# Kernel tuning notes

Hardware: AMD Instinct MI355X
Metric: run time of the kernel (lower is better)

The kernel has to match this reference:

```python
import jax, jax.numpy as jnp
import numpy as np

B, T, C = 4, 2048, 1024
N_HEAD = 16
HEAD_DIM = C // N_HEAD


def setup_inputs() -> dict:
    key = jax.random.key(0)
    ks = jax.random.split(key, 5)
    scale = 0.02
    return {
        "x": jax.random.normal(ks[0], (B, T, C), dtype=jnp.float32),
        "w_attn": jax.random.normal(ks[1], (C, 3 * C), dtype=jnp.float32) * scale,
        "b_attn": jax.random.normal(ks[2], (3 * C,), dtype=jnp.float32) * scale,
        "w_proj": jax.random.normal(ks[3], (C, C), dtype=jnp.float32) * scale,
        "b_proj": jax.random.normal(ks[4], (C,), dtype=jnp.float32) * scale,
    }


def reference(x, w_attn, b_attn, w_proj, b_proj):
    Bq, Tq, Cq = x.shape
    qkv = x @ w_attn + b_attn  # [B, T, 3C]
    q, k, v = jnp.split(qkv, 3, axis=2)
    # [B, H, T, D]
    q = q.reshape(Bq, Tq, N_HEAD, HEAD_DIM).transpose(0, 2, 1, 3)
    k = k.reshape(Bq, Tq, N_HEAD, HEAD_DIM).transpose(0, 2, 1, 3)
    v = v.reshape(Bq, Tq, N_HEAD, HEAD_DIM).transpose(0, 2, 1, 3)
    att = jnp.einsum("bhqd,bhkd->bhqk", q, k) * (HEAD_DIM ** -0.5)
    causal = jnp.tril(jnp.ones((Tq, Tq), dtype=bool))
    att = jnp.where(causal[None, None, :, :], att, -jnp.inf)
    att = jax.nn.softmax(att, axis=-1)
    out = jnp.einsum("bhqk,bhkd->bhqd", att, v)  # [B, H, T, D]
    out = out.transpose(0, 2, 1, 3).reshape(Bq, Tq, Cq)
    return out @ w_proj + b_proj
```

## Files before the change

kernel.cpp:

```cpp
#include <hip/hip_runtime.h>
#include <hip/hip_bf16.h>

#define Bsz 4
#define Tsz 2048
#define Csz 1024
#define NH  16
#define HD  64
#define NT  (Bsz * Tsz)

typedef unsigned short u16;
typedef unsigned int   u32;
typedef u16   u16x8  __attribute__((ext_vector_type(8)));
typedef u16   u16x4  __attribute__((ext_vector_type(4)));
typedef u32   u32x2  __attribute__((ext_vector_type(2)));
typedef short s16x8  __attribute__((ext_vector_type(8)));
typedef float f32x4  __attribute__((ext_vector_type(4)));

__device__ __forceinline__ float b2f(u16 u) {
    union { unsigned int i; float f; } x; x.i = ((unsigned int)u) << 16; return x.f;
}
__device__ __forceinline__ u16 f2b(float f) {
    unsigned int u = __float_as_uint(f);
    return (u16)((u + 0x7FFF + ((u >> 16) & 1)) >> 16);
}
__device__ __forceinline__ float ex2(float x) {
    float r; asm("v_exp_f32 %0, %1" : "=v"(r) : "v"(x)); return r;
}
__device__ __forceinline__ u32 cvtpk(float lo, float hi) {
    u32 r; asm("v_cvt_pk_bf16_f32 %0, %1, %2" : "=v"(r) : "v"(lo), "v"(hi)); return r;
}
__device__ __forceinline__ void gload16(const u16* g, u16* l) {
    __builtin_amdgcn_global_load_lds(
        (const __attribute__((address_space(1))) void*)g,
        (__attribute__((address_space(3))) void*)l, 16, 0, 0);
}

__global__ __launch_bounds__(256)
void conv_f32_bf16(const float* __restrict__ in, u16* __restrict__ out, int n8)
{
    int t = blockIdx.x * 256 + threadIdx.x;
    if (t >= n8) return;
    const float4* p = reinterpret_cast<const float4*>(in) + (size_t)t * 2;
    float4 a = p[0], b = p[1];
    u16x8 w;
    w[0] = f2b(a.x); w[1] = f2b(a.y); w[2] = f2b(a.z); w[3] = f2b(a.w);
    w[4] = f2b(b.x); w[5] = f2b(b.y); w[6] = f2b(b.z); w[7] = f2b(b.w);
    *(reinterpret_cast<u16x8*>(out) + t) = w;
}

__global__ __launch_bounds__(256)
void transpose_conv(const float* __restrict__ in, u16* __restrict__ out, int K, int N)
{
    __shared__ float tile[32][33];
    const int n0 = blockIdx.x * 32, k0 = blockIdx.y * 32;
    const int tx = threadIdx.x & 31, ty = threadIdx.x >> 5;
#pragma unroll
    for (int j = 0; j < 4; ++j)
        tile[ty + j * 8][tx] = in[(size_t)(k0 + ty + j * 8) * N + n0 + tx];
    __syncthreads();
#pragma unroll
    for (int j = 0; j < 4; ++j)
        out[(size_t)(n0 + ty + j * 8) * K + k0 + tx] = f2b(tile[tx][ty + j * 8]);
}

template<typename OutT>
__global__ __launch_bounds__(256)
void gemm_bf16(const u16* __restrict__ A, const u16* __restrict__ Bt,
               const float* __restrict__ bias, OutT* __restrict__ C,
               int M, int N, int K)
{
    __shared__ u16 As[128 * 64];
    __shared__ u16 Bs[128 * 64];

    const int tid  = threadIdx.x;
    const int lane = tid & 63;
    const int wid  = tid >> 6;
    const int wr   = wid >> 1;
    const int wc   = wid & 1;
    const int g    = lane >> 4;
    const int rr   = lane & 15;
    const int srow = lane >> 3;
    const int sslt = lane & 7;

    const int n0 = blockIdx.x * 128;
    const int m0 = blockIdx.y * 128;

    f32x4 acc[4][4];
#pragma unroll
    for (int m = 0; m < 4; ++m)
#pragma unroll
        for (int n = 0; n < 4; ++n) acc[m][n] = (f32x4){0.f, 0.f, 0.f, 0.f};

    for (int k0 = 0; k0 < K; k0 += 64) {
        __syncthreads();
#pragma unroll
        for (int p = 0; p < 4; ++p) {
            const int q = p * 4 + wid;
            const int r = q * 8 + srow;
            gload16(A  + (size_t)(m0 + r) * K + k0 + sslt * 8, &As[q * 512]);
            gload16(Bt + (size_t)(n0 + r) * K + k0 + sslt * 8, &Bs[q * 512]);
        }
        __syncthreads();

#pragma unroll
        for (int kk = 0; kk < 2; ++kk) {
            s16x8 af[4], bfr[4];
            const int s = kk * 4 + g;
#pragma unroll
            for (int m = 0; m < 4; ++m)
                af[m] = *reinterpret_cast<const s16x8*>(
                    &As[(wr * 64 + m * 16 + rr) * 64 + s * 8]);
#pragma unroll
            for (int n = 0; n < 4; ++n)
                bfr[n] = *reinterpret_cast<const s16x8*>(
                    &Bs[(wc * 64 + n * 16 + rr) * 64 + s * 8]);
#pragma unroll
            for (int m = 0; m < 4; ++m)
#pragma unroll
                for (int n = 0; n < 4; ++n)
                    acc[m][n] = __builtin_amdgcn_mfma_f32_16x16x32_bf16(
                        af[m], bfr[n], acc[m][n], 0, 0, 0);
        }
    }

#pragma unroll
    for (int m = 0; m < 4; ++m) {
#pragma unroll
        for (int n = 0; n < 4; ++n) {
            const int col = n0 + wc * 64 + n * 16 + rr;
            const float bv = bias[col];
#pragma unroll
            for (int j = 0; j < 4; ++j) {
                const int row = m0 + wr * 64 + m * 16 + g * 4 + j;
                const float v = acc[m][n][j] + bv;
                if constexpr (sizeof(OutT) == 2)
                    C[(size_t)row * N + col] = (OutT)f2b(v);
                else
                    C[(size_t)row * N + col] = (OutT)v;
            }
        }
    }
}

__global__ __launch_bounds__(256)
void attn_mfma(const u16* __restrict__ qkv, u16* __restrict__ out)
{
    __shared__ __align__(128) u16 Ks[64 * 64];
    __shared__ __align__(128) u16 Vt[64 * 64];
    __shared__ __align__(128) u16 Pl[4 * 2048];

    const int tid  = threadIdx.x;
    const int lane = tid & 63;
    const int wid  = tid >> 6;
    const int c    = lane & 15;
    const int g    = lane >> 4;

    const int bh = blockIdx.x;
    const int b  = bh >> 4;
    const int h  = bh & 15;
    const int skey = tid >> 3;
    const int sb   = tid & 7;
    const u32 pbyte = ((u32)(size_t)(&Pl[0])) + wid * 4096 + lane * 8;
    const float QSC = 0.18033688f;

    for (int half = 0; half < 2; ++half) {
        const int yt = half ? 15 - (int)blockIdx.y : (int)blockIdx.y;
        const int t0 = yt * 128;
        const int qb0 = t0 + wid * 32;

        s16x8 qf[2][2];
#pragma unroll
        for (int m = 0; m < 2; ++m)
#pragma unroll
            for (int kk = 0; kk < 2; ++kk) {
                u16x8 raw = *reinterpret_cast<const u16x8*>(
                    qkv + (size_t)(b * Tsz + qb0 + m * 16 + c) * (3 * Csz)
                        + h * HD + kk * 32 + g * 8);
                s16x8 qv;
#pragma unroll
                for (int i = 0; i < 8; ++i) qv[i] = (short)f2b(b2f(raw[i]) * QSC);
                qf[m][kk] = qv;
            }

        f32x4 acco[2][4];
#pragma unroll
        for (int m = 0; m < 2; ++m)
#pragma unroll
            for (int dn = 0; dn < 4; ++dn) acco[m][dn] = (f32x4){0.f, 0.f, 0.f, 0.f};
        float mrun[8], lrun[8];
#pragma unroll
        for (int i = 0; i < 8; ++i) { mrun[i] = -1e30f; lrun[i] = 0.f; }

        for (int kt = 0; kt < t0 + 128; kt += 64) {
#pragma unroll
            for (int p = 0; p < 2; ++p) {
                const int key = skey + p * 32;
                const u16* gk = qkv + (size_t)(b * Tsz + kt + key) * (3 * Csz)
                                + Csz + h * HD + sb * 8;
                u16x8 kv = *reinterpret_cast<const u16x8*>(gk);
                u16x8 vv = *reinterpret_cast<const u16x8*>(gk + Csz);
                *reinterpret_cast<u16x8*>(&Ks[key * 64 + ((sb ^ (key & 7)) * 8)]) = kv;
#pragma unroll
                for (int i = 0; i < 8; ++i) {
                    const int d = sb * 8 + i;
                    Vt[d * 64 + (key ^ (((i ^ sb) & 7) << 3))] = vv[i];
                }
            }
            __syncthreads();

            if (kt <= qb0 + 31) {
                f32x4 accS[2][4];
#pragma unroll
                for (int m = 0; m < 2; ++m)
#pragma unroll
                    for (int n = 0; n < 4; ++n) accS[m][n] = (f32x4){0.f, 0.f, 0.f, 0.f};
#pragma unroll
                for (int kk = 0; kk < 2; ++kk) {
                    s16x8 kf[4];
#pragma unroll
                    for (int n = 0; n < 4; ++n) {
                        const int key = n * 16 + c;
                        kf[n] = *reinterpret_cast<const s16x8*>(
                            &Ks[key * 64 + (((kk * 4 + g) ^ (c & 7)) * 8)]);
                    }
#pragma unroll
                    for (int m = 0; m < 2; ++m)
#pragma unroll
                        for (int n = 0; n < 4; ++n)
                            accS[m][n] = __builtin_amdgcn_mfma_f32_16x16x32_bf16(
                                qf[m][kk], kf[n], accS[m][n], 0, 0, 0);
                }

                if (kt + 63 > qb0) {
#pragma unroll
                    for (int m = 0; m < 2; ++m)
#pragma unroll
                        for (int n = 0; n < 4; ++n) {
                            const int kgl = kt + n * 16 + c;
#pragma unroll
                            for (int j = 0; j < 4; ++j) {
                                const int qg = qb0 + m * 16 + g * 4 + j;
                                if (kgl > qg) accS[m][n][j] = -1e30f;
                            }
                        }
                }

                float pm[8];
#pragma unroll
                for (int m = 0; m < 2; ++m)
#pragma unroll
                    for (int j = 0; j < 4; ++j)
                        pm[m * 4 + j] = fmaxf(fmaxf(accS[m][0][j], accS[m][1][j]),
                                              fmaxf(accS[m][2][j], accS[m][3][j]));
#pragma unroll
                for (int msk = 1; msk < 16; msk <<= 1)
#pragma unroll
                    for (int i = 0; i < 8; ++i)
                        pm[i] = fmaxf(pm[i], __shfl_xor(pm[i], msk));

                int need = 0;
#pragma unroll
                for (int i = 0; i < 8; ++i) need |= (pm[i] > mrun[i] + 8.f);
                if (__any(need)) {
                    float cvec[8];
#pragma unroll
                    for (int i = 0; i < 8; ++i) {
                        const float mn = fmaxf(mrun[i], pm[i]);
                        cvec[i] = ex2(mrun[i] - mn);
                        mrun[i] = mn;
                        lrun[i] *= cvec[i];
                    }
#pragma unroll
                    for (int m = 0; m < 2; ++m)
#pragma unroll
                        for (int dn = 0; dn < 4; ++dn)
#pragma unroll
                            for (int j = 0; j < 4; ++j)
                                acco[m][dn][j] *= cvec[m * 4 + j];
                }

#pragma unroll
                for (int m = 0; m < 2; ++m)
#pragma unroll
                    for (int n = 0; n < 4; ++n) {
                        float pv[4];
#pragma unroll
                        for (int j = 0; j < 4; ++j) {
                            pv[j] = ex2(accS[m][n][j] - mrun[m * 4 + j]);
                            lrun[m * 4 + j] += pv[j];
                        }
                        const u32 w0 = cvtpk(pv[0], pv[1]);
                        const u32 w1 = cvtpk(pv[2], pv[3]);
                        const int slot = (n >> 1) * 32 + ((c >> 2) & 1) * 16
                                       + ((n & 1) * 2 + (c >> 3)) * 4 + (c & 3);
                        *reinterpret_cast<u32x2*>(
                            &Pl[wid * 2048 + m * 1024 + slot * 16 + g * 4]) = (u32x2){w0, w1};
                    }
                asm volatile("s_waitcnt lgkmcnt(0)" ::: "memory");
                __builtin_amdgcn_sched_barrier(0);

                u16x4 t000, t001, t010, t011, t100, t101, t110, t111;
                asm volatile("ds_read_b64_tr_b16 %0, %1"             : "=v"(t000) : "v"(pbyte));
                asm volatile("ds_read_b64_tr_b16 %0, %1 offset:512"  : "=v"(t001) : "v"(pbyte));
                asm volatile("ds_read_b64_tr_b16 %0, %1 offset:1024" : "=v"(t010) : "v"(pbyte));
                asm volatile("ds_read_b64_tr_b16 %0, %1 offset:1536" : "=v"(t011) : "v"(pbyte));
                asm volatile("ds_read_b64_tr_b16 %0, %1 offset:2048" : "=v"(t100) : "v"(pbyte));
                asm volatile("ds_read_b64_tr_b16 %0, %1 offset:2560" : "=v"(t101) : "v"(pbyte));
                asm volatile("ds_read_b64_tr_b16 %0, %1 offset:3072" : "=v"(t110) : "v"(pbyte));
                asm volatile("ds_read_b64_tr_b16 %0, %1 offset:3584" : "=v"(t111) : "v"(pbyte));
                asm volatile("s_waitcnt lgkmcnt(0)" ::: "memory");
                __builtin_amdgcn_sched_barrier(0);

                s16x8 pa[2][2];
#pragma unroll
                for (int q = 0; q < 4; ++q) {
                    pa[0][0][q] = (short)t000[q]; pa[0][0][q + 4] = (short)t001[q];
                    pa[0][1][q] = (short)t010[q]; pa[0][1][q + 4] = (short)t011[q];
                    pa[1][0][q] = (short)t100[q]; pa[1][0][q + 4] = (short)t101[q];
                    pa[1][1][q] = (short)t110[q]; pa[1][1][q + 4] = (short)t111[q];
                }

#pragma unroll
                for (int kk = 0; kk < 2; ++kk) {
                    s16x8 vf[4];
#pragma unroll
                    for (int dn = 0; dn < 4; ++dn) {
                        const int d = dn * 16 + c;
                        const int swz = (c & 7) ^ ((dn * 2 + (c >> 3)) & 7);
                        vf[dn] = *reinterpret_cast<const s16x8*>(
                            &Vt[d * 64 + (((kk * 4 + g) ^ swz) * 8)]);
                    }
#pragma unroll
                    for (int m = 0; m < 2; ++m)
#pragma unroll
                        for (int dn = 0; dn < 4; ++dn)
                            acco[m][dn] = __builtin_amdgcn_mfma_f32_16x16x32_bf16(
                                pa[m][kk], vf[dn], acco[m][dn], 0, 0, 0);
                }
            }
            __syncthreads();
        }

#pragma unroll
        for (int msk = 1; msk < 16; msk <<= 1)
#pragma unroll
            for (int i = 0; i < 8; ++i)
                lrun[i] += __shfl_xor(lrun[i], msk);
        float inv[8];
#pragma unroll
        for (int i = 0; i < 8; ++i) inv[i] = 1.f / lrun[i];
#pragma unroll
        for (int m = 0; m < 2; ++m)
#pragma unroll
            for (int dn = 0; dn < 4; ++dn)
#pragma unroll
                for (int j = 0; j < 4; ++j) {
                    const int q = qb0 + m * 16 + g * 4 + j;
                    out[(size_t)(b * Tsz + q) * Csz + h * HD + dn * 16 + c] =
                        f2b(acco[m][dn][j] * inv[m * 4 + j]);
                }
    }
}

extern "C" void kernel_launch(void* const* d_in, const int* in_sizes, int n_in,
                              void* d_out, int out_size, void* d_ws, size_t ws_size,
                              hipStream_t stream) {
    const float* x      = (const float*)d_in[0];
    const float* w_attn = (const float*)d_in[1];
    const float* b_attn = (const float*)d_in[2];
    const float* w_proj = (const float*)d_in[3];
    const float* b_proj = (const float*)d_in[4];
    float* out = (float*)d_out;

    char* w = (char*)d_ws;
    u16* qkv_bf = (u16*)w;  w += (size_t)NT * 3 * Csz * 2;
    u16* x_bf   = (u16*)w;  w += (size_t)NT * Csz * 2;
    u16* ao_bf  = (u16*)w;  w += (size_t)NT * Csz * 2;
    u16* wat    = (u16*)w;  w += (size_t)3 * Csz * Csz * 2;
    u16* wpt    = (u16*)w;

    conv_f32_bf16<<<(NT * Csz / 8 + 255) / 256, 256, 0, stream>>>(x, x_bf, NT * Csz / 8);
    transpose_conv<<<dim3(3 * Csz / 32, Csz / 32), 256, 0, stream>>>(w_attn, wat, Csz, 3 * Csz);
    transpose_conv<<<dim3(Csz / 32, Csz / 32), 256, 0, stream>>>(w_proj, wpt, Csz, Csz);

    gemm_bf16<u16><<<dim3(3 * Csz / 128, NT / 128), 256, 0, stream>>>(
        x_bf, wat, b_attn, qkv_bf, NT, 3 * Csz, Csz);

    attn_mfma<<<dim3(Bsz * NH, 8), 256, 0, stream>>>(qkv_bf, ao_bf);

    gemm_bf16<float><<<dim3(Csz / 128, NT / 128), 256, 0, stream>>>(
        ao_bf, wpt, b_proj, out, NT, Csz, Csz);
}
```

Baseline: 299.9 us.

## Fuse x conversion into QKV GEMM, remap blocks, widen attention key tiles

Drops the separate fp32-to-bf16 conversion kernel for x. The QKV GEMM now loads fp32 x into registers, packs it to bf16 and writes it to LDS itself. Both GEMMs remap workgroup IDs in a strided pattern, aimed at L2/cache locality. The attention kernel moves to 128-key tiles, register-prefetches the next K/V tile during compute, stores V untransposed and reads it with ds_read_b64_tr_b16, and applies the causal mask only on the diagonal tile. These changes raise LDS usage and register pressure, and the A-operand path for the first GEMM is no longer async.

New measurement: 322.0 us. +7.4%, slower.

```diff
diff --git a/kernel.cpp b/kernel.cpp
--- a/kernel.cpp
+++ b/kernel.cpp
@@ -13,6 +13,7 @@
 typedef u16   u16x8  __attribute__((ext_vector_type(8)));
 typedef u16   u16x4  __attribute__((ext_vector_type(4)));
 typedef u32   u32x2  __attribute__((ext_vector_type(2)));
+typedef u32   u32x4  __attribute__((ext_vector_type(4)));
 typedef short s16x8  __attribute__((ext_vector_type(8)));
 typedef float f32x4  __attribute__((ext_vector_type(4)));
 
@@ -34,19 +35,19 @@
         (const __attribute__((address_space(1))) void*)g,
         (__attribute__((address_space(3))) void*)l, 16, 0, 0);
 }
-
-__global__ __launch_bounds__(256)
-void conv_f32_bf16(const float* __restrict__ in, u16* __restrict__ out, int n8)
-{
-    int t = blockIdx.x * 256 + threadIdx.x;
-    if (t >= n8) return;
-    const float4* p = reinterpret_cast<const float4*>(in) + (size_t)t * 2;
-    float4 a = p[0], b = p[1];
-    u16x8 w;
-    w[0] = f2b(a.x); w[1] = f2b(a.y); w[2] = f2b(a.z); w[3] = f2b(a.w);
-    w[4] = f2b(b.x); w[5] = f2b(b.y); w[6] = f2b(b.z); w[7] = f2b(b.w);
-    *(reinterpret_cast<u16x8*>(out) + t) = w;
-}
+__device__ __forceinline__ void tr8(u32 a, u16x4 t[8]) {
+    asm volatile("ds_read_b64_tr_b16 %0, %1"             : "=v"(t[0]) : "v"(a));
+    asm volatile("ds_read_b64_tr_b16 %0, %1 offset:512"  : "=v"(t[1]) : "v"(a));
+    asm volatile("ds_read_b64_tr_b16 %0, %1 offset:1024" : "=v"(t[2]) : "v"(a));
+    asm volatile("ds_read_b64_tr_b16 %0, %1 offset:1536" : "=v"(t[3]) : "v"(a));
+    asm volatile("ds_read_b64_tr_b16 %0, %1 offset:2048" : "=v"(t[4]) : "v"(a));
+    asm volatile("ds_read_b64_tr_b16 %0, %1 offset:2560" : "=v"(t[5]) : "v"(a));
+    asm volatile("ds_read_b64_tr_b16 %0, %1 offset:3072" : "=v"(t[6]) : "v"(a));
+    asm volatile("ds_read_b64_tr_b16 %0, %1 offset:3584" : "=v"(t[7]) : "v"(a));
+}
+#define LGKM0_FENCE() do { \
+    asm volatile("s_waitcnt lgkmcnt(0)" ::: "memory"); \
+    __builtin_amdgcn_sched_barrier(0); } while (0)
 
 __global__ __launch_bounds__(256)
 void transpose_conv(const float* __restrict__ in, u16* __restrict__ out, int K, int N)
@@ -63,9 +64,9 @@
         out[(size_t)(n0 + ty + j * 8) * K + k0 + tx] = f2b(tile[tx][ty + j * 8]);
 }
 
-template<typename OutT>
+template<typename AT, typename OutT>
 __global__ __launch_bounds__(256)
-void gemm_bf16(const u16* __restrict__ A, const u16* __restrict__ Bt,
+void gemm_bf16(const AT* __restrict__ A, const u16* __restrict__ Bt,
                const float* __restrict__ bias, OutT* __restrict__ C,
                int M, int N, int K)
 {
@@ -82,8 +83,11 @@
     const int srow = lane >> 3;
     const int sslt = lane & 7;
 
-    const int n0 = blockIdx.x * 128;
-    const int m0 = blockIdx.y * 128;
+    const int nwg = (int)(gridDim.x * gridDim.y);
+    int fid = (int)(blockIdx.y * gridDim.x + blockIdx.x);
+    fid = (fid & 7) * (nwg >> 3) + (fid >> 3);
+    const int n0 = (fid % (int)gridDim.x) * 128;
+    const int m0 = (fid / (int)gridDim.x) * 128;
 
     f32x4 acc[4][4];
 #pragma unroll
@@ -92,13 +96,34 @@
         for (int n = 0; n < 4; ++n) acc[m][n] = (f32x4){0.f, 0.f, 0.f, 0.f};
 
     for (int k0 = 0; k0 < K; k0 += 64) {
+        float4 a0[4], a1[4];
+        if constexpr (sizeof(AT) == 4) {
+#pragma unroll
+            for (int p = 0; p < 4; ++p) {
+                const int r = (p * 4 + wid) * 8 + srow;
+                const float* ap = (const float*)A + (size_t)(m0 + r) * K + k0 + sslt * 8;
+                a0[p] = *reinterpret_cast<const float4*>(ap);
+                a1[p] = *reinterpret_cast<const float4*>(ap + 4);
+            }
+        }
         __syncthreads();
 #pragma unroll
         for (int p = 0; p < 4; ++p) {
             const int q = p * 4 + wid;
             const int r = q * 8 + srow;
-            gload16(A  + (size_t)(m0 + r) * K + k0 + sslt * 8, &As[q * 512]);
             gload16(Bt + (size_t)(n0 + r) * K + k0 + sslt * 8, &Bs[q * 512]);
+            if constexpr (sizeof(AT) == 2)
+                gload16((const u16*)A + (size_t)(m0 + r) * K + k0 + sslt * 8, &As[q * 512]);
+        }
+        if constexpr (sizeof(AT) == 4) {
+#pragma unroll
+            for (int p = 0; p < 4; ++p) {
+                const int q = p * 4 + wid;
+                u32x4 w;
+                w[0] = cvtpk(a0[p].x, a0[p].y); w[1] = cvtpk(a0[p].z, a0[p].w);
+                w[2] = cvtpk(a1[p].x, a1[p].y); w[3] = cvtpk(a1[p].z, a1[p].w);
+                *reinterpret_cast<u32x4*>(&As[q * 512 + lane * 8]) = w;
+            }
         }
         __syncthreads();
 
@@ -145,9 +170,9 @@
 __global__ __launch_bounds__(256)
 void attn_mfma(const u16* __restrict__ qkv, u16* __restrict__ out)
 {
-    __shared__ __align__(128) u16 Ks[64 * 64];
-    __shared__ __align__(128) u16 Vt[64 * 64];
-    __shared__ __align__(128) u16 Pl[4 * 2048];
+    __shared__ __align__(128) u16 Ks[128 * 64];
+    __shared__ __align__(128) u16 Vl[4 * 2048];
+    __shared__ __align__(128) u16 Pl[4 * 4096];
 
     const int tid  = threadIdx.x;
     const int lane = tid & 63;
@@ -158,14 +183,33 @@
     const int bh = blockIdx.x;
     const int b  = bh >> 4;
     const int h  = bh & 15;
+
     const int skey = tid >> 3;
     const int sb   = tid & 7;
-    const u32 pbyte = ((u32)(size_t)(&Pl[0])) + wid * 4096 + lane * 8;
+    const int kswz = (sb ^ (skey & 7)) * 8;
+    const int vslotb = ((skey >> 2) & 1) * 16 + (((skey >> 4) & 1) * 2 + ((skey >> 3) & 1)) * 4
+                     + (skey & 3);
+    const int vaddr0 = (sb >> 1) * 2048 + vslotb * 16 + (sb & 1) * 8;
+    const int slotc  = ((c >> 2) & 1) * 16 + (c >> 3) * 4 + (c & 3);
+
+    const u32 pbyte = ((u32)(size_t)(&Pl[0])) + wid * 8192 + lane * 8;
+    const u32 vbyte = ((u32)(size_t)(&Vl[0])) + lane * 8;
     const float QSC = 0.18033688f;
 
+    u16x8 kreg[4], vreg[4];
+    const u16* kvbase = qkv + (size_t)b * Tsz * (3 * Csz) + Csz + h * HD + sb * 8;
+    auto load_kv = [&](int kt) {
+#pragma unroll
+        for (int p = 0; p < 4; ++p) {
+            const u16* gk = kvbase + (size_t)(kt + skey + p * 32) * (3 * Csz);
+            kreg[p] = *reinterpret_cast<const u16x8*>(gk);
+            vreg[p] = *reinterpret_cast<const u16x8*>(gk + Csz);
+        }
+    };
+
     for (int half = 0; half < 2; ++half) {
-        const int yt = half ? 15 - (int)blockIdx.y : (int)blockIdx.y;
-        const int t0 = yt * 128;
+        const int yt  = half ? 15 - (int)blockIdx.y : (int)blockIdx.y;
+        const int t0  = yt * 128;
         const int qb0 = t0 + wid * 32;
 
         s16x8 qf[2][2];
@@ -191,57 +235,52 @@
 #pragma unroll
         for (int i = 0; i < 8; ++i) { mrun[i] = -1e30f; lrun[i] = 0.f; }
 
-        for (int kt = 0; kt < t0 + 128; kt += 64) {
-#pragma unroll
-            for (int p = 0; p < 2; ++p) {
-                const int key = skey + p * 32;
-                const u16* gk = qkv + (size_t)(b * Tsz + kt + key) * (3 * Csz)
-                                + Csz + h * HD + sb * 8;
-                u16x8 kv = *reinterpret_cast<const u16x8*>(gk);
-                u16x8 vv = *reinterpret_cast<const u16x8*>(gk + Csz);
-                *reinterpret_cast<u16x8*>(&Ks[key * 64 + ((sb ^ (key & 7)) * 8)]) = kv;
-#pragma unroll
-                for (int i = 0; i < 8; ++i) {
-                    const int d = sb * 8 + i;
-                    Vt[d * 64 + (key ^ (((i ^ sb) & 7) << 3))] = vv[i];
-                }
-            }
+        load_kv(0);
+
+        for (int kt = 0; kt < t0 + 128; kt += 128) {
             __syncthreads();
-
-            if (kt <= qb0 + 31) {
-                f32x4 accS[2][4];
+#pragma unroll
+            for (int p = 0; p < 4; ++p) {
+                *reinterpret_cast<u16x8*>(&Ks[(skey + p * 32) * 64 + kswz]) = kreg[p];
+                *reinterpret_cast<u16x8*>(&Vl[vaddr0 + p * 512]) = vreg[p];
+            }
+            if (kt < t0) load_kv(kt + 128);
+            __syncthreads();
+
+            {
+                f32x4 accS[2][8];
 #pragma unroll
                 for (int m = 0; m < 2; ++m)
 #pragma unroll
-                    for (int n = 0; n < 4; ++n) accS[m][n] = (f32x4){0.f, 0.f, 0.f, 0.f};
-#pragma unroll
-                for (int kk = 0; kk < 2; ++kk) {
-                    s16x8 kf[4];
-#pragma unroll
-                    for (int n = 0; n < 4; ++n) {
-                        const int key = n * 16 + c;
-                        kf[n] = *reinterpret_cast<const s16x8*>(
-                            &Ks[key * 64 + (((kk * 4 + g) ^ (c & 7)) * 8)]);
+                    for (int n = 0; n < 8; ++n) accS[m][n] = (f32x4){0.f, 0.f, 0.f, 0.f};
+#pragma unroll
+                for (int kk = 0; kk < 2; ++kk)
+#pragma unroll
+                    for (int nh = 0; nh < 2; ++nh) {
+                        s16x8 kf[4];
+#pragma unroll
+                        for (int i = 0; i < 4; ++i) {
+                            const int key = (nh * 4 + i) * 16 + c;
+                            kf[i] = *reinterpret_cast<const s16x8*>(
+                                &Ks[key * 64 + (((kk * 4 + g) ^ (c & 7)) * 8)]);
+                        }
+#pragma unroll
+                        for (int m = 0; m < 2; ++m)
+#pragma unroll
+                            for (int i = 0; i < 4; ++i)
+                                accS[m][nh * 4 + i] = __builtin_amdgcn_mfma_f32_16x16x32_bf16(
+                                    qf[m][kk], kf[i], accS[m][nh * 4 + i], 0, 0, 0);
                     }
+
+                if (kt == t0) {
 #pragma unroll
                     for (int m = 0; m < 2; ++m)
 #pragma unroll
-                        for (int n = 0; n < 4; ++n)
-                            accS[m][n] = __builtin_amdgcn_mfma_f32_16x16x32_bf16(
-                                qf[m][kk], kf[n], accS[m][n], 0, 0, 0);
-                }
-
-                if (kt + 63 > qb0) {
-#pragma unroll
-                    for (int m = 0; m < 2; ++m)
-#pragma unroll
-                        for (int n = 0; n < 4; ++n) {
+                        for (int n = 0; n < 8; ++n) {
                             const int kgl = kt + n * 16 + c;
 #pragma unroll
-                            for (int j = 0; j < 4; ++j) {
-                                const int qg = qb0 + m * 16 + g * 4 + j;
-                                if (kgl > qg) accS[m][n][j] = -1e30f;
-                            }
+                            for (int j = 0; j < 4; ++j)
+                                if (kgl > qb0 + m * 16 + g * 4 + j) accS[m][n][j] = -1e30f;
                         }
                 }
 
@@ -249,9 +288,12 @@
 #pragma unroll
                 for (int m = 0; m < 2; ++m)
 #pragma unroll
-                    for (int j = 0; j < 4; ++j)
-                        pm[m * 4 + j] = fmaxf(fmaxf(accS[m][0][j], accS[m][1][j]),
-                                              fmaxf(accS[m][2][j], accS[m][3][j]));
+                    for (int j = 0; j < 4; ++j) {
+                        float v = accS[m][0][j];
+#pragma unroll
+                        for (int n = 1; n < 8; ++n) v = fmaxf(v, accS[m][n][j]);
+                        pm[m * 4 + j] = v;
+                    }
 #pragma unroll
                 for (int msk = 1; msk < 16; msk <<= 1)
 #pragma unroll
@@ -262,13 +304,13 @@
 #pragma unroll
                 for (int i = 0; i < 8; ++i) need |= (pm[i] > mrun[i] + 8.f);
                 if (__any(need)) {
-                    float cvec[8];
+                    float cv[8];
 #pragma unroll
                     for (int i = 0; i < 8; ++i) {
                         const float mn = fmaxf(mrun[i], pm[i]);
-                        cvec[i] = ex2(mrun[i] - mn);
+                        cv[i] = ex2(mrun[i] - mn);
                         mrun[i] = mn;
-                        lrun[i] *= cvec[i];
+                        lrun[i] *= cv[i];
                     }
 #pragma unroll
                     for (int m = 0; m < 2; ++m)
@@ -276,69 +318,62 @@
                         for (int dn = 0; dn < 4; ++dn)
 #pragma unroll
                             for (int j = 0; j < 4; ++j)
-                                acco[m][dn][j] *= cvec[m * 4 + j];
+                                acco[m][dn][j] *= cv[m * 4 + j];
                 }
 
 #pragma unroll
                 for (int m = 0; m < 2; ++m)
 #pragma unroll
-                    for (int n = 0; n < 4; ++n) {
+                    for (int n = 0; n < 8; ++n) {
                         float pv[4];
 #pragma unroll
                         for (int j = 0; j < 4; ++j) {
                             pv[j] = ex2(accS[m][n][j] - mrun[m * 4 + j]);
                             lrun[m * 4 + j] += pv[j];
                         }
-                        const u32 w0 = cvtpk(pv[0], pv[1]);
-                        const u32 w1 = cvtpk(pv[2], pv[3]);
-                        const int slot = (n >> 1) * 32 + ((c >> 2) & 1) * 16
-                                       + ((n & 1) * 2 + (c >> 3)) * 4 + (c & 3);
+                        const int slot = (n >> 1) * 32 + (n & 1) * 8 + slotc;
                         *reinterpret_cast<u32x2*>(
-                            &Pl[wid * 2048 + m * 1024 + slot * 16 + g * 4]) = (u32x2){w0, w1};
+                            &Pl[wid * 4096 + m * 2048 + slot * 16 + g * 4]) =
+                            (u32x2){cvtpk(pv[0], pv[1]), cvtpk(pv[2], pv[3])};
                     }
-                asm volatile("s_waitcnt lgkmcnt(0)" ::: "memory");
-                __builtin_amdgcn_sched_barrier(0);
-
-                u16x4 t000, t001, t010, t011, t100, t101, t110, t111;
-                asm volatile("ds_read_b64_tr_b16 %0, %1"             : "=v"(t000) : "v"(pbyte));
-                asm volatile("ds_read_b64_tr_b16 %0, %1 offset:512"  : "=v"(t001) : "v"(pbyte));
-                asm volatile("ds_read_b64_tr_b16 %0, %1 offset:1024" : "=v"(t010) : "v"(pbyte));
-                asm volatile("ds_read_b64_tr_b16 %0, %1 offset:1536" : "=v"(t011) : "v"(pbyte));
-                asm volatile("ds_read_b64_tr_b16 %0, %1 offset:2048" : "=v"(t100) : "v"(pbyte));
-                asm volatile("ds_read_b64_tr_b16 %0, %1 offset:2560" : "=v"(t101) : "v"(pbyte));
-                asm volatile("ds_read_b64_tr_b16 %0, %1 offset:3072" : "=v"(t110) : "v"(pbyte));
-                asm volatile("ds_read_b64_tr_b16 %0, %1 offset:3584" : "=v"(t111) : "v"(pbyte));
-                asm volatile("s_waitcnt lgkmcnt(0)" ::: "memory");
-                __builtin_amdgcn_sched_barrier(0);
-
-                s16x8 pa[2][2];
-#pragma unroll
-                for (int q = 0; q < 4; ++q) {
-                    pa[0][0][q] = (short)t000[q]; pa[0][0][q + 4] = (short)t001[q];
-                    pa[0][1][q] = (short)t010[q]; pa[0][1][q + 4] = (short)t011[q];
-                    pa[1][0][q] = (short)t100[q]; pa[1][0][q + 4] = (short)t101[q];
-                    pa[1][1][q] = (short)t110[q]; pa[1][1][q + 4] = (short)t111[q];
+                LGKM0_FENCE();
+
+                u16x4 tp0[8], tp1[8];
+                tr8(pbyte, tp0);
+                tr8(pbyte + 4096, tp1);
+                LGKM0_FENCE();
+                s16x8 pa[2][4];
+#pragma unroll
+                for (int K32 = 0; K32 < 4; ++K32)
+#pragma unroll
+                    for (int q = 0; q < 4; ++q) {
+                        pa[0][K32][q] = (short)tp0[K32 * 2][q];
+                        pa[0][K32][q + 4] = (short)tp0[K32 * 2 + 1][q];
+                        pa[1][K32][q] = (short)tp1[K32 * 2][q];
+                        pa[1][K32][q + 4] = (short)tp1[K32 * 2 + 1][q];
+                    }
+
+#pragma unroll
+                for (int dn = 0; dn < 4; ++dn) {
+                    u16x4 tv[8];
+                    tr8(vbyte + dn * 4096, tv);
+                    LGKM0_FENCE();
+                    s16x8 vfk[4];
+#pragma unroll
+                    for (int K32 = 0; K32 < 4; ++K32)
+#pragma unroll
+                        for (int q = 0; q < 4; ++q) {
+                            vfk[K32][q] = (short)tv[K32 * 2][q];
+                            vfk[K32][q + 4] = (short)tv[K32 * 2 + 1][q];
+                        }
+#pragma unroll
+                    for (int m = 0; m < 2; ++m)
+#pragma unroll
+                        for (int K32 = 0; K32 < 4; ++K32)
+                            acco[m][dn] = __builtin_amdgcn_mfma_f32_16x16x32_bf16(
+                                pa[m][K32], vfk[K32], acco[m][dn], 0, 0, 0);
                 }
-
-#pragma unroll
-                for (int kk = 0; kk < 2; ++kk) {
-                    s16x8 vf[4];
-#pragma unroll
-                    for (int dn = 0; dn < 4; ++dn) {
-                        const int d = dn * 16 + c;
-                        const int swz = (c & 7) ^ ((dn * 2 + (c >> 3)) & 7);
-                        vf[dn] = *reinterpret_cast<const s16x8*>(
-                            &Vt[d * 64 + (((kk * 4 + g) ^ swz) * 8)]);
-                    }
-#pragma unroll
-                    for (int m = 0; m < 2; ++m)
-#pragma unroll
-                        for (int dn = 0; dn < 4; ++dn)
-                            acco[m][dn] = __builtin_amdgcn_mfma_f32_16x16x32_bf16(
-                                pa[m][kk], vf[dn], acco[m][dn], 0, 0, 0);
-                }
-            }
-            __syncthreads();
+            }
         }
 
 #pragma unroll
@@ -359,6 +394,7 @@
                     out[(size_t)(b * Tsz + q) * Csz + h * HD + dn * 16 + c] =
                         f2b(acco[m][dn][j] * inv[m * 4 + j]);
                 }
+        __syncthreads();
     }
 }
 
@@ -374,20 +410,18 @@
 
     char* w = (char*)d_ws;
     u16* qkv_bf = (u16*)w;  w += (size_t)NT * 3 * Csz * 2;
-    u16* x_bf   = (u16*)w;  w += (size_t)NT * Csz * 2;
     u16* ao_bf  = (u16*)w;  w += (size_t)NT * Csz * 2;
     u16* wat    = (u16*)w;  w += (size_t)3 * Csz * Csz * 2;
     u16* wpt    = (u16*)w;
 
-    conv_f32_bf16<<<(NT * Csz / 8 + 255) / 256, 256, 0, stream>>>(x, x_bf, NT * Csz / 8);
     transpose_conv<<<dim3(3 * Csz / 32, Csz / 32), 256, 0, stream>>>(w_attn, wat, Csz, 3 * Csz);
     transpose_conv<<<dim3(Csz / 32, Csz / 32), 256, 0, stream>>>(w_proj, wpt, Csz, Csz);
 
-    gemm_bf16<u16><<<dim3(3 * Csz / 128, NT / 128), 256, 0, stream>>>(
-        x_bf, wat, b_attn, qkv_bf, NT, 3 * Csz, Csz);
+    gemm_bf16<float, u16><<<dim3(3 * Csz / 128, NT / 128), 256, 0, stream>>>(
+        x, wat, b_attn, qkv_bf, NT, 3 * Csz, Csz);
 
     attn_mfma<<<dim3(Bsz * NH, 8), 256, 0, stream>>>(qkv_bf, ao_bf);
 
-    gemm_bf16<float><<<dim3(Csz / 128, NT / 128), 256, 0, stream>>>(
+    gemm_bf16<u16, float><<<dim3(Csz / 128, NT / 128), 256, 0, stream>>>(
         ao_bf, wpt, b_proj, out, NT, Csz, Csz);
 }
```
